# Kernel optimization log

Hardware: AMD Instinct MI355X
Metric: run time of the kernel (lower is better)

## Reference

```python
import jax, jax.numpy as jnp
import numpy as np

BS, T, N, M, P = 1024, 128, 128, 256, 256


def _lstm_cell(xin, h, c, Wih, Whh, bih, bhh):
    # PyTorch LSTMCell: gates ordered i, f, g, o
    z = xin @ Wih.T + bih + h @ Whh.T + bhh
    i, f, g, o = jnp.split(z, 4, axis=1)
    i = jax.nn.sigmoid(i); f = jax.nn.sigmoid(f)
    g = jnp.tanh(g); o = jax.nn.sigmoid(o)
    c2 = f * c + i * g
    return o * jnp.tanh(c2), c2


def setup_inputs() -> dict:
    key = jax.random.key(0)
    ks = jax.random.split(key, 24)
    s = 0.05
    return {
        "x": jax.random.normal(ks[0], (BS, T, N), jnp.float32),
        "y_known": jax.random.normal(ks[1], (BS, T, 1), jnp.float32),
        "We": jax.random.normal(ks[2], (T, 2 * M), jnp.float32) * s,
        "Ue": jax.random.normal(ks[3], (T, T), jnp.float32) * s,
        "Ve": jax.random.normal(ks[4], (1, T), jnp.float32) * s,
        "Wih_e": jax.random.normal(ks[5], (4 * M, N), jnp.float32) * s,
        "Whh_e": jax.random.normal(ks[6], (4 * M, M), jnp.float32) * s,
        "bih_e": jax.random.normal(ks[7], (4 * M,), jnp.float32) * s,
        "bhh_e": jax.random.normal(ks[8], (4 * M,), jnp.float32) * s,
        "Wd": jax.random.normal(ks[9], (M, 2 * P), jnp.float32) * s,
        "Ud": jax.random.normal(ks[10], (M, M), jnp.float32) * s,
        "Vd": jax.random.normal(ks[11], (1, M), jnp.float32) * s,
        "Wih_d": jax.random.normal(ks[12], (4 * P, 1), jnp.float32) * s,
        "Whh_d": jax.random.normal(ks[13], (4 * P, P), jnp.float32) * s,
        "bih_d": jax.random.normal(ks[14], (4 * P,), jnp.float32) * s,
        "bhh_d": jax.random.normal(ks[15], (4 * P,), jnp.float32) * s,
        "Wt": jax.random.normal(ks[16], (1, M + 1), jnp.float32) * s,
        "bt": jax.random.normal(ks[17], (1,), jnp.float32) * s,
        "W1": jax.random.normal(ks[18], (P, P + M), jnp.float32) * s,
        "b1": jax.random.normal(ks[19], (P,), jnp.float32) * s,
        "W2": jax.random.normal(ks[20], (1, P), jnp.float32) * s,
        "b2": jax.random.normal(ks[21], (1,), jnp.float32) * s,
    }


def reference(x, y_known, We, Ue, Ve, Wih_e, Whh_e, bih_e, bhh_e,
              Wd, Ud, Vd, Wih_d, Whh_d, bih_d, bhh_d,
              Wt, bt, W1, b1, W2, b2):
    bs, Tl, n = x.shape
    m = Whh_e.shape[1]
    p = Whh_d.shape[1]

    # ---- encoder (input attention) ----
    # U_e(x.permute(0,2,1)): loop-invariant, hoisted. (bs, n, T)
    Ux = jnp.einsum('btn,st->bns', x, Ue)

    def enc_step(carry, _):
        h, s = carry
        hs = jnp.concatenate([h, s], axis=1)            # (bs, 2m)
        ohs = hs @ We.T                                  # (bs, T)
        tanh_sum = jnp.tanh(ohs[:, None, :] + Ux)        # (bs, n, T)
        e = jnp.einsum('bnt,t->bn', tanh_sum, Ve[0])     # (bs, n)
        alpha = jax.nn.softmax(e, axis=1)
        xt = alpha * e                                   # faithful quirk: alpha * e_t
        h2, s2 = _lstm_cell(xt, h, s, Wih_e, Whh_e, bih_e, bhh_e)
        return (h2, s2), h2

    z = jnp.zeros((bs, m), x.dtype)
    _, h_all = jax.lax.scan(enc_step, (z, z), None, length=Tl)
    x1 = jnp.transpose(h_all, (1, 2, 0))                 # (bs, m, T)

    # ---- decoder (temporal attention) ----
    Udx = jnp.einsum('bmt,km->btk', x1, Ud)              # (bs, T, m)

    def dec_step(carry, yt):
        d, s, _ = carry
        ds = jnp.concatenate([d, s], axis=1)             # (bs, 2p)
        ods = ds @ Wd.T                                   # (bs, m)
        tanh_sum = jnp.tanh(ods[:, None, :] + Udx)        # (bs, T, m)
        l = jnp.einsum('btm,m->bt', tanh_sum, Vd[0])      # (bs, T)
        beta = jax.nn.softmax(l, axis=1)
        c = jnp.einsum('bt,bmt->bm', beta, x1)            # (bs, m)
        y_tilde = jnp.concatenate([yt, c], axis=1) @ Wt.T + bt  # (bs, 1)
        d2, s2 = _lstm_cell(y_tilde, d, s, Wih_d, Whh_d, bih_d, bhh_d)
        return (d2, s2, c), None

    zp = jnp.zeros((bs, p), x.dtype)
    zc = jnp.zeros((bs, m), x.dtype)
    (d, _, c), _ = jax.lax.scan(dec_step, (zp, zp, zc),
                                jnp.transpose(y_known, (1, 0, 2)))
    out1 = jnp.concatenate([d, c], axis=1) @ W1.T + b1
    return out1 @ W2.T + b2
```

## Files before the change

kernel.cpp:

```cpp
#include <hip/hip_runtime.h>


typedef unsigned int   uint;
typedef unsigned short ushort;
typedef _Float16 h2v __attribute__((ext_vector_type(2)));

#define O_WEH     0u
#define O_WENCH   32768u
#define O_WDH     229376u
#define O_WHHDH   294912u
#define O_UDT     425984u
#define O_UET     491520u
#define O_W1T     507904u
#define O_BENC    638976u
#define O_BDEC    640000u
#define W_FLOATS  641024u
#define O_X1H     641024u
#define O_BUF     17418240u
#define WS_FLOATS 34195456u

#define C2E 2.8853900817779268f
#define L2E 1.4426950408889634f

#define FMA4(acc, s, w) \
  acc.x = fmaf((s), (w).x, acc.x); \
  acc.y = fmaf((s), (w).y, acc.y); \
  acc.z = fmaf((s), (w).z, acc.z); \
  acc.w = fmaf((s), (w).w, acc.w);

union H2U { uint u; h2v h; _Float16 hs[2]; };

__device__ __forceinline__ float fdot2u(uint w, uint s, float acc) {
  H2U a; a.u = w; H2U b; b.u = s;
  return __builtin_amdgcn_fdot2(a.h, b.h, acc, false);
}
__device__ __forceinline__ uint pk2(float lo, float hi) {
  H2U v; v.hs[0] = (_Float16)lo; v.hs[1] = (_Float16)hi; return v.u;
}
__device__ __forceinline__ float h2lo(uint u) { H2U v; v.u = u; return (float)v.hs[0]; }
__device__ __forceinline__ float h2hi(uint u) { H2U v; v.u = u; return (float)v.hs[1]; }

__device__ __forceinline__ float fsig(float x) {
  return __builtin_amdgcn_rcpf(1.f + __builtin_amdgcn_exp2f(-L2E * x));
}
__device__ __forceinline__ float fth(float x) {
  float r = __builtin_amdgcn_rcpf(1.f + __builtin_amdgcn_exp2f(C2E * x));
  return fmaf(-2.f, r, 1.f);
}

__device__ __forceinline__ float grp4_sum(float v, float* red) {
  #pragma unroll
  for (int o = 32; o > 0; o >>= 1) v += __shfl_xor(v, o);
  __syncthreads();
  int w = threadIdx.x >> 6;
  if ((threadIdx.x & 63) == 0) red[w] = v;
  __syncthreads();
  int wb = w & 4;
  return (red[wb] + red[wb + 1]) + (red[wb + 2] + red[wb + 3]);
}
__device__ __forceinline__ float grp4_max(float v, float* red) {
  #pragma unroll
  for (int o = 32; o > 0; o >>= 1) v = fmaxf(v, __shfl_xor(v, o));
  __syncthreads();
  int w = threadIdx.x >> 6;
  if ((threadIdx.x & 63) == 0) red[w] = v;
  __syncthreads();
  int wb = w & 4;
  return fmaxf(fmaxf(red[wb], red[wb + 1]), fmaxf(red[wb + 2], red[wb + 3]));
}

__global__ __launch_bounds__(256) void prep_k(
    const float* __restrict__ We,    const float* __restrict__ Wih_e,
    const float* __restrict__ Whh_e, const float* __restrict__ Wd,
    const float* __restrict__ Whh_d, const float* __restrict__ W1,
    const float* __restrict__ Ud,    const float* __restrict__ Ue,
    const float* __restrict__ bih_e, const float* __restrict__ bhh_e,
    const float* __restrict__ bih_d, const float* __restrict__ bhh_d,
    float* __restrict__ ws)
{
  uint* wsu = (uint*)ws;
  unsigned idx = blockIdx.x * 256u + threadIdx.x;
  if (idx >= W_FLOATS) return;
  if (idx < 32768u) {
    unsigned kp = idx >> 7, j = idx & 127u;
    wsu[O_WEH + idx] = pk2(We[j * 512u + 2u*kp], We[j * 512u + 2u*kp + 1u]);
  } else if (idx < 229376u) {
    unsigned rel = idx - 32768u;
    unsigned kp = rel >> 10, j = rel & 1023u;
    float v0, v1;
    if (kp < 64u) { v0 = Wih_e[j * 128u + 2u*kp];          v1 = Wih_e[j * 128u + 2u*kp + 1u]; }
    else { unsigned k0 = 2u*(kp - 64u); v0 = Whh_e[j * 256u + k0]; v1 = Whh_e[j * 256u + k0 + 1u]; }
    wsu[O_WENCH + rel] = pk2(v0, v1);
  } else if (idx < 294912u) {
    unsigned rel = idx - 229376u;
    unsigned kp = rel >> 8, kk = rel & 255u;
    wsu[O_WDH + rel] = pk2(Wd[kk * 512u + 2u*kp], Wd[kk * 512u + 2u*kp + 1u]);
  } else if (idx < 425984u) {
    unsigned rel = idx - 294912u;
    unsigned kp = rel >> 10, j = rel & 1023u;
    wsu[O_WHHDH + rel] = pk2(Whh_d[j * 256u + 2u*kp], Whh_d[j * 256u + 2u*kp + 1u]);
  } else if (idx < 491520u) {
    unsigned rel = idx - 425984u;
    unsigned m = rel >> 8, k = rel & 255u;
    ws[O_UDT + rel] = Ud[k * 256u + m];
  } else if (idx < 507904u) {
    unsigned rel = idx - 491520u;
    unsigned t = rel >> 7, s = rel & 127u;
    ws[O_UET + rel] = Ue[s * 128u + t];
  } else if (idx < 638976u) {
    unsigned rel = idx - 507904u;
    unsigned k = rel >> 8, q = rel & 255u;
    ws[O_W1T + rel] = W1[q * 512u + k];
  } else if (idx < 640000u) {
    unsigned rel = idx - 638976u;
    ws[O_BENC + rel] = bih_e[rel] + bhh_e[rel];
  } else {
    unsigned rel = idx - 640000u;
    ws[O_BDEC + rel] = bih_d[rel] + bhh_d[rel];
  }
}

__global__ __launch_bounds__(256) void ux_k(
    const float* __restrict__ x, const float* __restrict__ UeT,
    uint* __restrict__ UxU)
{
  __shared__ float xs[128][32];
  const int b  = blockIdx.x >> 2;
  const int i0 = (blockIdx.x & 3) * 32;
  const int tid = threadIdx.x;
  for (int idx = tid; idx < 4096; idx += 256) {
    int t = idx >> 5, il = idx & 31;
    xs[t][il] = x[(size_t)b * 16384 + t * 128 + i0 + il];
  }
  __syncthreads();
  const int sl = tid & 31;
  const int ig = tid >> 5;
  const float4* UeT4 = (const float4*)UeT;
  float4 acc[4];
  #pragma unroll
  for (int ii = 0; ii < 4; ++ii) acc[ii] = make_float4(0.f, 0.f, 0.f, 0.f);
  for (int t = 0; t < 128; ++t) {
    float4 w = UeT4[t * 32 + sl];
    #pragma unroll
    for (int ii = 0; ii < 4; ++ii) {
      float a = xs[t][ig + 8 * ii];
      FMA4(acc[ii], a, w);
    }
  }
  uint2* U2 = (uint2*)UxU;
  #pragma unroll
  for (int ii = 0; ii < 4; ++ii) {
    int i_loc = i0 + ig + 8 * ii;
    uint2 pk;
    pk.x = pk2(acc[ii].x, acc[ii].y);
    pk.y = pk2(acc[ii].z, acc[ii].w);
    U2[((size_t)b * 128 + i_loc) * 32 + sl] = pk;
  }
}

__global__ __launch_bounds__(256) void udx_k(
    const uint* __restrict__ x1hU, const float* __restrict__ UdT,
    uint* __restrict__ UdxU)
{
  __shared__ float xs[32][256];
  const int b  = blockIdx.x >> 2;
  const int t0 = (blockIdx.x & 3) * 32;
  const int tid = threadIdx.x;
  const uint4* x14 = (const uint4*)x1hU + (size_t)b * 4096;
  for (int it = 0; it < 4; ++it) {
    int f = tid + it * 256;
    int tl = f >> 5, mq = f & 31;
    uint4 u = x14[(size_t)(t0 + tl) * 32 + mq];
    float* d = &xs[tl][mq * 8];
    d[0] = h2lo(u.x); d[1] = h2hi(u.x); d[2] = h2lo(u.y); d[3] = h2hi(u.y);
    d[4] = h2lo(u.z); d[5] = h2hi(u.z); d[6] = h2lo(u.w); d[7] = h2hi(u.w);
  }
  __syncthreads();
  const int kl = tid & 63;
  const int tg = tid >> 6;
  const float4* UdT4 = (const float4*)UdT;
  float4 acc[8];
  #pragma unroll
  for (int tt = 0; tt < 8; ++tt) acc[tt] = make_float4(0.f, 0.f, 0.f, 0.f);
  for (int m = 0; m < 256; ++m) {
    float4 w = UdT4[m * 64 + kl];
    #pragma unroll
    for (int tt = 0; tt < 8; ++tt) {
      float a = xs[tg + 4 * tt][m];
      FMA4(acc[tt], a, w);
    }
  }
  uint2* U2 = (uint2*)UdxU;
  #pragma unroll
  for (int tt = 0; tt < 8; ++tt) {
    uint2 pk;
    pk.x = pk2(acc[tt].x, acc[tt].y);
    pk.y = pk2(acc[tt].z, acc[tt].w);
    U2[((size_t)b * 128 + t0 + tg + 4 * tt) * 64 + kl] = pk;
  }
}

__global__ __launch_bounds__(512, 4) void encoder_k(
    const uint* __restrict__ WeH, const uint* __restrict__ WencH,
    const float* __restrict__ benc, const float* __restrict__ Ve,
    const uint* __restrict__ UxH, uint* __restrict__ x1hU)
{
  __shared__ uint stH[2][256];
  __shared__ uint xtH[2][64];
  __shared__ __align__(16) float part[4096];
  __shared__ float ohs2[2][128];
  __shared__ float xtT[128][2];
  __shared__ float bencS[1024];
  __shared__ float VeS[128];
  __shared__ float red[8];

  const int tid = threadIdx.x;
  const int b0 = blockIdx.x * 2;

  ((uint*)stH)[tid] = 0u;
  for (int i = tid; i < 1024; i += 512) bencS[i] = benc[i];
  if (tid < 128) VeS[tid] = Ve[tid];
  __syncthreads();

  float SVe = 0.f;
  #pragma unroll 8
  for (int s = 0; s < 128; ++s) SVe += VeS[s];

  const uint4* WeH4   = (const uint4*)WeH;
  const uint4* WencH4 = (const uint4*)WencH;
  float4* part4 = (float4*)part;

  const int rB = tid >> 8, iB = (tid >> 1) & 127, sh = tid & 1;
  const uint4* ux4 = (const uint4*)UxH + ((size_t)(b0 + rB) * 128 + iB) * 16 + sh * 8;

  float c_reg = 0.f;

  for (int step = 0; step < 128; ++step) {
    {
      const int j4 = tid & 31, ks = tid >> 5;
      float a0=0,a1=0,a2=0,a3=0,b0=0,b1=0,b2=0,b3=0;
      const int kb = ks * 16;
      #pragma unroll 4
      for (int kp = kb; kp < kb + 16; ++kp) {
        uint4 w = WeH4[kp * 32 + j4];
        uint s0 = stH[0][kp], s1 = stH[1][kp];
        a0 = fdot2u(w.x, s0, a0); a1 = fdot2u(w.y, s0, a1);
        a2 = fdot2u(w.z, s0, a2); a3 = fdot2u(w.w, s0, a3);
        b0 = fdot2u(w.x, s1, b0); b1 = fdot2u(w.y, s1, b1);
        b2 = fdot2u(w.z, s1, b2); b3 = fdot2u(w.w, s1, b3);
      }
      part4[(ks * 2 + 0) * 32 + j4] = make_float4(a0, a1, a2, a3);
      part4[(ks * 2 + 1) * 32 + j4] = make_float4(b0, b1, b2, b3);
    }
    __syncthreads();
    if (tid < 256) {
      const int r = tid >> 7, j = tid & 127;
      float acc = 0.f;
      #pragma unroll
      for (int ks = 0; ks < 16; ++ks) acc += part[(ks * 2 + r) * 128 + j];
      ohs2[r][j] = acc * C2E;
    }
    __syncthreads();
    float e_val;
    {
      float a0 = 0.f, a1 = 0.f, a2 = 0.f, a3 = 0.f;
      const float* oh = ohs2[rB];
      #pragma unroll 2
      for (int so = 0; so < 8; ++so) {
        uint4 u = ux4[so];
        const int s = sh * 64 + so * 8;
        a0 = fmaf(VeS[s+0], __builtin_amdgcn_rcpf(1.f + __builtin_amdgcn_exp2f(fmaf(C2E, h2lo(u.x), oh[s+0]))), a0);
        a1 = fmaf(VeS[s+1], __builtin_amdgcn_rcpf(1.f + __builtin_amdgcn_exp2f(fmaf(C2E, h2hi(u.x), oh[s+1]))), a1);
        a2 = fmaf(VeS[s+2], __builtin_amdgcn_rcpf(1.f + __builtin_amdgcn_exp2f(fmaf(C2E, h2lo(u.y), oh[s+2]))), a2);
        a3 = fmaf(VeS[s+3], __builtin_amdgcn_rcpf(1.f + __builtin_amdgcn_exp2f(fmaf(C2E, h2hi(u.y), oh[s+3]))), a3);
        a0 = fmaf(VeS[s+4], __builtin_amdgcn_rcpf(1.f + __builtin_amdgcn_exp2f(fmaf(C2E, h2lo(u.z), oh[s+4]))), a0);
        a1 = fmaf(VeS[s+5], __builtin_amdgcn_rcpf(1.f + __builtin_amdgcn_exp2f(fmaf(C2E, h2hi(u.z), oh[s+5]))), a1);
        a2 = fmaf(VeS[s+6], __builtin_amdgcn_rcpf(1.f + __builtin_amdgcn_exp2f(fmaf(C2E, h2lo(u.w), oh[s+6]))), a2);
        a3 = fmaf(VeS[s+7], __builtin_amdgcn_rcpf(1.f + __builtin_amdgcn_exp2f(fmaf(C2E, h2hi(u.w), oh[s+7]))), a3);
      }
      float r4 = (a0 + a1) + (a2 + a3);
      r4 += __shfl_xor(r4, 1);
      e_val = fmaf(-2.f, r4, SVe);
    }
    float mx = grp4_max(e_val, red);
    float p  = __builtin_amdgcn_exp2f(L2E * (e_val - mx));
    float sm = grp4_sum(sh == 0 ? p : 0.f, red);
    if (sh == 0) xtT[iB][rB] = p * __builtin_amdgcn_rcpf(sm) * e_val;
    __syncthreads();
    if (tid < 128) {
      const int r = tid >> 6, ii = tid & 63;
      xtH[r][ii] = pk2(xtT[2 * ii][r], xtT[2 * ii + 1][r]);
    }
    __syncthreads();
    {
      const int j4 = tid & 255, ks = tid >> 8;
      float a0=0,a1=0,a2=0,a3=0,b0=0,b1=0,b2=0,b3=0;
      if (ks == 0) {
        #pragma unroll 2
        for (int kp = 0; kp < 64; ++kp) {
          uint4 w = WencH4[kp * 256 + j4];
          uint s0 = xtH[0][kp], s1 = xtH[1][kp];
          a0 = fdot2u(w.x, s0, a0); a1 = fdot2u(w.y, s0, a1);
          a2 = fdot2u(w.z, s0, a2); a3 = fdot2u(w.w, s0, a3);
          b0 = fdot2u(w.x, s1, b0); b1 = fdot2u(w.y, s1, b1);
          b2 = fdot2u(w.z, s1, b2); b3 = fdot2u(w.w, s1, b3);
        }
        #pragma unroll 2
        for (int kp = 64; kp < 96; ++kp) {
          uint4 w = WencH4[kp * 256 + j4];
          uint s0 = stH[0][kp - 64], s1 = stH[1][kp - 64];
          a0 = fdot2u(w.x, s0, a0); a1 = fdot2u(w.y, s0, a1);
          a2 = fdot2u(w.z, s0, a2); a3 = fdot2u(w.w, s0, a3);
          b0 = fdot2u(w.x, s1, b0); b1 = fdot2u(w.y, s1, b1);
          b2 = fdot2u(w.z, s1, b2); b3 = fdot2u(w.w, s1, b3);
        }
      } else {
        #pragma unroll 2
        for (int kp = 96; kp < 192; ++kp) {
          uint4 w = WencH4[kp * 256 + j4];
          uint s0 = stH[0][kp - 64], s1 = stH[1][kp - 64];
          a0 = fdot2u(w.x, s0, a0); a1 = fdot2u(w.y, s0, a1);
          a2 = fdot2u(w.z, s0, a2); a3 = fdot2u(w.w, s0, a3);
          b0 = fdot2u(w.x, s1, b0); b1 = fdot2u(w.y, s1, b1);
          b2 = fdot2u(w.z, s1, b2); b3 = fdot2u(w.w, s1, b3);
        }
      }
      part4[(ks * 2 + 0) * 256 + j4] = make_float4(a0, a1, a2, a3);
      part4[(ks * 2 + 1) * 256 + j4] = make_float4(b0, b1, b2, b3);
    }
    __syncthreads();
    {
      const int r = tid >> 8, j = tid & 255;
      float z0 = bencS[j]       + part[r * 1024 + j]       + part[(2 + r) * 1024 + j];
      float z1 = bencS[256 + j] + part[r * 1024 + 256 + j] + part[(2 + r) * 1024 + 256 + j];
      float z2 = bencS[512 + j] + part[r * 1024 + 512 + j] + part[(2 + r) * 1024 + 512 + j];
      float z3 = bencS[768 + j] + part[r * 1024 + 768 + j] + part[(2 + r) * 1024 + 768 + j];
      float gi = fsig(z0), gf = fsig(z1), gg = fth(z2), go = fsig(z3);
      float c2 = fmaf(gf, c_reg, gi * gg);
      c_reg = c2;
      float h2 = go * fth(c2);
      float hn = __shfl_down(h2, 1);
      float cn = __shfl_down(c2, 1);
      if (!(j & 1)) {
        uint hp = pk2(h2, hn), cp = pk2(c2, cn);
        stH[r][j >> 1] = hp;
        stH[r][128 + (j >> 1)] = cp;
        x1hU[((size_t)(b0 + r) * 128 + step) * 128 + (j >> 1)] = hp;
      }
    }
    __syncthreads();
  }
}

__global__ __launch_bounds__(512, 4) void decoder_k(
    const uint* __restrict__ WdH, const uint* __restrict__ WhhdH,
    const float* __restrict__ W1T, const float* __restrict__ bdec,
    const float* __restrict__ Vd,  const float* __restrict__ WihD,
    const float* __restrict__ Wt,  const float* __restrict__ btp,
    const float* __restrict__ b1,  const float* __restrict__ W2,
    const float* __restrict__ b2p, const float* __restrict__ yk,
    const uint* __restrict__ UdxH, const uint* __restrict__ x1hU,
    float* __restrict__ out)
{
  __shared__ uint stH[2][256];
  __shared__ __align__(16) float part[4096];
  __shared__ float ods2[2][256];
  __shared__ float cT[256][2];
  __shared__ float betaT[128][2];
  __shared__ float wihdS[1024];
  __shared__ float bdecS[1024];
  __shared__ float VdS[256];
  __shared__ float yts[2];
  __shared__ float red[8];

  const int tid = threadIdx.x;
  const int b0 = blockIdx.x * 2;

  ((uint*)stH)[tid] = 0u;
  for (int i = tid; i < 1024; i += 512) { wihdS[i] = WihD[i]; bdecS[i] = bdec[i]; }
  if (tid < 256) VdS[tid] = Vd[tid];
  __syncthreads();

  float SVd = 0.f;
  #pragma unroll 8
  for (int k = 0; k < 256; ++k) SVd += VdS[k];

  const float bt0 = btp[0];
  const uint4*  WdH4   = (const uint4*)WdH;
  const uint4*  WhhdH4 = (const uint4*)WhhdH;
  const float4* W1T4   = (const float4*)W1T;
  float4* part4 = (float4*)part;

  const int rB = tid >> 8, tB = (tid >> 1) & 127, kh = tid & 1;
  const uint4* ud4 = (const uint4*)UdxH + ((size_t)(b0 + rB) * 128 + tB) * 32 + kh * 16;
  const int m8 = tid & 31, rb2 = (tid >> 5) & 1, ts = tid >> 6;
  const uint4* x14 = (const uint4*)x1hU + (size_t)(b0 + rb2) * 4096 + m8;

  float c_reg = 0.f;

  for (int step = 0; step < 128; ++step) {
    {
      const int j4 = tid & 63, ks = tid >> 6;
      float a0=0,a1=0,a2=0,a3=0,b0=0,b1=0,b2=0,b3=0;
      const int kb = ks * 32;
      #pragma unroll 4
      for (int kp = kb; kp < kb + 32; ++kp) {
        uint4 w = WdH4[kp * 64 + j4];
        uint s0 = stH[0][kp], s1 = stH[1][kp];
        a0 = fdot2u(w.x, s0, a0); a1 = fdot2u(w.y, s0, a1);
        a2 = fdot2u(w.z, s0, a2); a3 = fdot2u(w.w, s0, a3);
        b0 = fdot2u(w.x, s1, b0); b1 = fdot2u(w.y, s1, b1);
        b2 = fdot2u(w.z, s1, b2); b3 = fdot2u(w.w, s1, b3);
      }
      part4[(ks * 2 + 0) * 64 + j4] = make_float4(a0, a1, a2, a3);
      part4[(ks * 2 + 1) * 64 + j4] = make_float4(b0, b1, b2, b3);
    }
    __syncthreads();
    {
      const int r = tid >> 8, kk = tid & 255;
      float acc = 0.f;
      #pragma unroll
      for (int ks = 0; ks < 8; ++ks) acc += part[(ks * 2 + r) * 256 + kk];
      ods2[r][kk] = acc * C2E;
    }
    __syncthreads();
    float l_val;
    {
      float a0 = 0.f, a1 = 0.f, a2 = 0.f, a3 = 0.f;
      const float* od = ods2[rB];
      #pragma unroll 2
      for (int ko = 0; ko < 16; ++ko) {
        uint4 u = ud4[ko];
        const int k = kh * 128 + ko * 8;
        a0 = fmaf(VdS[k+0], __builtin_amdgcn_rcpf(1.f + __builtin_amdgcn_exp2f(fmaf(C2E, h2lo(u.x), od[k+0]))), a0);
        a1 = fmaf(VdS[k+1], __builtin_amdgcn_rcpf(1.f + __builtin_amdgcn_exp2f(fmaf(C2E, h2hi(u.x), od[k+1]))), a1);
        a2 = fmaf(VdS[k+2], __builtin_amdgcn_rcpf(1.f + __builtin_amdgcn_exp2f(fmaf(C2E, h2lo(u.y), od[k+2]))), a2);
        a3 = fmaf(VdS[k+3], __builtin_amdgcn_rcpf(1.f + __builtin_amdgcn_exp2f(fmaf(C2E, h2hi(u.y), od[k+3]))), a3);
        a0 = fmaf(VdS[k+4], __builtin_amdgcn_rcpf(1.f + __builtin_amdgcn_exp2f(fmaf(C2E, h2lo(u.z), od[k+4]))), a0);
        a1 = fmaf(VdS[k+5], __builtin_amdgcn_rcpf(1.f + __builtin_amdgcn_exp2f(fmaf(C2E, h2hi(u.z), od[k+5]))), a1);
        a2 = fmaf(VdS[k+6], __builtin_amdgcn_rcpf(1.f + __builtin_amdgcn_exp2f(fmaf(C2E, h2lo(u.w), od[k+6]))), a2);
        a3 = fmaf(VdS[k+7], __builtin_amdgcn_rcpf(1.f + __builtin_amdgcn_exp2f(fmaf(C2E, h2hi(u.w), od[k+7]))), a3);
      }
      float r4 = (a0 + a1) + (a2 + a3);
      r4 += __shfl_xor(r4, 1);
      l_val = fmaf(-2.f, r4, SVd);
    }
    float mx = grp4_max(l_val, red);
    float p  = __builtin_amdgcn_exp2f(L2E * (l_val - mx));
    float sm = grp4_sum(kh == 0 ? p : 0.f, red);
    if (kh == 0) betaT[tB][rB] = p * __builtin_amdgcn_rcpf(sm);
    __syncthreads();
    {
      float c[8];
      #pragma unroll
      for (int e = 0; e < 8; ++e) c[e] = 0.f;
      #pragma unroll 4
      for (int tt = 0; tt < 16; ++tt) {
        const int t = ts * 16 + tt;
        float bv = betaT[t][rb2];
        uint4 u = x14[(size_t)t * 32];
        c[0] = fmaf(bv, h2lo(u.x), c[0]); c[1] = fmaf(bv, h2hi(u.x), c[1]);
        c[2] = fmaf(bv, h2lo(u.y), c[2]); c[3] = fmaf(bv, h2hi(u.y), c[3]);
        c[4] = fmaf(bv, h2lo(u.z), c[4]); c[5] = fmaf(bv, h2hi(u.z), c[5]);
        c[6] = fmaf(bv, h2lo(u.w), c[6]); c[7] = fmaf(bv, h2hi(u.w), c[7]);
      }
      part4[(ts * 2 + rb2) * 64 + m8 * 2]     = make_float4(c[0], c[1], c[2], c[3]);
      part4[(ts * 2 + rb2) * 64 + m8 * 2 + 1] = make_float4(c[4], c[5], c[6], c[7]);
    }
    __syncthreads();
    {
      const int r = tid >> 8, m = tid & 255;
      float v = 0.f;
      #pragma unroll
      for (int t8 = 0; t8 < 8; ++t8) v += part[(t8 * 2 + r) * 256 + m];
      cT[m][r] = v;
    }
    __syncthreads();
    {
      const int r = tid >> 8, i = tid & 255;
      float pv = cT[i][r] * Wt[1 + i];
      float sum = grp4_sum(pv, red);
      if ((tid & 255) == 0) {
        yts[r] = sum + yk[(size_t)(b0 + r) * 128 + step] * Wt[0] + bt0;
      }
    }
    {
      const int j4 = tid & 255, ks = tid >> 8;
      float a0=0,a1=0,a2=0,a3=0,b0=0,b1=0,b2=0,b3=0;
      const int kb = ks * 64;
      #pragma unroll 2
      for (int kp = kb; kp < kb + 64; ++kp) {
        uint4 w = WhhdH4[kp * 256 + j4];
        uint s0 = stH[0][kp], s1 = stH[1][kp];
        a0 = fdot2u(w.x, s0, a0); a1 = fdot2u(w.y, s0, a1);
        a2 = fdot2u(w.z, s0, a2); a3 = fdot2u(w.w, s0, a3);
        b0 = fdot2u(w.x, s1, b0); b1 = fdot2u(w.y, s1, b1);
        b2 = fdot2u(w.z, s1, b2); b3 = fdot2u(w.w, s1, b3);
      }
      part4[(ks * 2 + 0) * 256 + j4] = make_float4(a0, a1, a2, a3);
      part4[(ks * 2 + 1) * 256 + j4] = make_float4(b0, b1, b2, b3);
    }
    __syncthreads();
    {
      const int r = tid >> 8, j = tid & 255;
      float yt = yts[r];
      float z0 = fmaf(yt, wihdS[j],       bdecS[j])       + part[r * 1024 + j]       + part[(2 + r) * 1024 + j];
      float z1 = fmaf(yt, wihdS[256 + j], bdecS[256 + j]) + part[r * 1024 + 256 + j] + part[(2 + r) * 1024 + 256 + j];
      float z2 = fmaf(yt, wihdS[512 + j], bdecS[512 + j]) + part[r * 1024 + 512 + j] + part[(2 + r) * 1024 + 512 + j];
      float z3 = fmaf(yt, wihdS[768 + j], bdecS[768 + j]) + part[r * 1024 + 768 + j] + part[(2 + r) * 1024 + 768 + j];
      float gi = fsig(z0), gf = fsig(z1), gg = fth(z2), go = fsig(z3);
      float c2 = fmaf(gf, c_reg, gi * gg);
      c_reg = c2;
      float d2 = go * fth(c2);
      float dn = __shfl_down(d2, 1);
      float cn = __shfl_down(c2, 1);
      if (!(j & 1)) {
        stH[r][j >> 1] = pk2(d2, dn);
        stH[r][128 + (j >> 1)] = pk2(c2, cn);
      }
    }
    __syncthreads();
  }
  {
    const int l = tid & 63, ks = tid >> 6;
    float a0=0,a1=0,a2=0,a3=0,b0=0,b1=0,b2=0,b3=0;
    const int kb = ks * 64;
    if (ks < 4) {
      for (int k = kb; k < kb + 64; ++k) {
        float4 w = W1T4[k * 64 + l];
        uint u0 = stH[0][k >> 1], u1 = stH[1][k >> 1];
        float d0 = (k & 1) ? h2hi(u0) : h2lo(u0);
        float d1 = (k & 1) ? h2hi(u1) : h2lo(u1);
        a0=fmaf(d0,w.x,a0); a1=fmaf(d0,w.y,a1); a2=fmaf(d0,w.z,a2); a3=fmaf(d0,w.w,a3);
        b0=fmaf(d1,w.x,b0); b1=fmaf(d1,w.y,b1); b2=fmaf(d1,w.z,b2); b3=fmaf(d1,w.w,b3);
      }
    } else {
      for (int k = kb; k < kb + 64; ++k) {
        float4 w = W1T4[k * 64 + l];
        float c0 = cT[k - 256][0], c1 = cT[k - 256][1];
        a0=fmaf(c0,w.x,a0); a1=fmaf(c0,w.y,a1); a2=fmaf(c0,w.z,a2); a3=fmaf(c0,w.w,a3);
        b0=fmaf(c1,w.x,b0); b1=fmaf(c1,w.y,b1); b2=fmaf(c1,w.z,b2); b3=fmaf(c1,w.w,b3);
      }
    }
    part4[(ks * 2 + 0) * 64 + l] = make_float4(a0, a1, a2, a3);
    part4[(ks * 2 + 1) * 64 + l] = make_float4(b0, b1, b2, b3);
  }
  __syncthreads();
  {
    const int r = tid >> 8, q = tid & 255;
    float o1 = b1[q];
    #pragma unroll
    for (int ks = 0; ks < 8; ++ks) o1 += part[(ks * 2 + r) * 256 + q];
    float pv = o1 * W2[q];
    float sum = grp4_sum(pv, red);
    if ((tid & 255) == 0) out[b0 + r] = sum + b2p[0];
  }
}

extern "C" void kernel_launch(void* const* d_in, const int* in_sizes, int n_in,
                              void* d_out, int out_size, void* d_ws, size_t ws_size,
                              hipStream_t stream)
{
  const float* x       = (const float*)d_in[0];
  const float* y_known = (const float*)d_in[1];
  const float* We      = (const float*)d_in[2];
  const float* Ue      = (const float*)d_in[3];
  const float* Ve      = (const float*)d_in[4];
  const float* Wih_e   = (const float*)d_in[5];
  const float* Whh_e   = (const float*)d_in[6];
  const float* bih_e   = (const float*)d_in[7];
  const float* bhh_e   = (const float*)d_in[8];
  const float* Wd      = (const float*)d_in[9];
  const float* Ud      = (const float*)d_in[10];
  const float* Vd      = (const float*)d_in[11];
  const float* Wih_d   = (const float*)d_in[12];
  const float* Whh_d   = (const float*)d_in[13];
  const float* bih_d   = (const float*)d_in[14];
  const float* bhh_d   = (const float*)d_in[15];
  const float* Wt      = (const float*)d_in[16];
  const float* bt      = (const float*)d_in[17];
  const float* W1      = (const float*)d_in[18];
  const float* b1      = (const float*)d_in[19];
  const float* W2      = (const float*)d_in[20];
  const float* b2      = (const float*)d_in[21];

  float* ws  = (float*)d_ws;
  float* out = (float*)d_out;
  if (ws_size < (size_t)WS_FLOATS * 4u) return;

  uint* wsu  = (uint*)ws;
  uint* x1hU = (uint*)(ws + O_X1H);
  uint* bufU = (uint*)(ws + O_BUF);

  prep_k<<<(W_FLOATS + 255) / 256, 256, 0, stream>>>(
      We, Wih_e, Whh_e, Wd, Whh_d, W1, Ud, Ue,
      bih_e, bhh_e, bih_d, bhh_d, ws);

  ux_k<<<4096, 256, 0, stream>>>(x, ws + O_UET, bufU);
  encoder_k<<<512, 512, 0, stream>>>(wsu + O_WEH, wsu + O_WENCH,
                                     ws + O_BENC, Ve, bufU, x1hU);
  udx_k<<<4096, 256, 0, stream>>>(x1hU, ws + O_UDT, bufU);
  decoder_k<<<512, 512, 0, stream>>>(wsu + O_WDH, wsu + O_WHHDH,
                                     ws + O_W1T, ws + O_BDEC, Vd, Wih_d,
                                     Wt, bt, b1, W2, b2, y_known,
                                     bufU, x1hU, out);
}
```

Before: 7.281 ms.

## Double encoder/decoder block threads and drop softmax max reduction

Encoder and decoder recurrent kernels now run with 1024 threads per block instead of 512. Every matvec and attention stage is re-split to give each thread half the work, with padded shared arrays to avoid bank conflicts. The softmax max-subtraction pass is removed, which saves one block-wide reduction per step but relies on the logits being small enough not to overflow exp. Several barrier pairs are merged, for example by fusing the context reduction with the y_tilde dot product. The cost is more partial-sum traffic through shared memory and more threads waiting at each barrier.

```diff
diff --git a/kernel.cpp b/kernel.cpp
--- a/kernel.cpp
+++ b/kernel.cpp
@@ -48,26 +48,11 @@
   return fmaf(-2.f, r, 1.f);
 }
 
-__device__ __forceinline__ float grp4_sum(float v, float* red) {
-  #pragma unroll
-  for (int o = 32; o > 0; o >>= 1) v += __shfl_xor(v, o);
-  __syncthreads();
-  int w = threadIdx.x >> 6;
-  if ((threadIdx.x & 63) == 0) red[w] = v;
-  __syncthreads();
-  int wb = w & 4;
-  return (red[wb] + red[wb + 1]) + (red[wb + 2] + red[wb + 3]);
-}
-__device__ __forceinline__ float grp4_max(float v, float* red) {
-  #pragma unroll
-  for (int o = 32; o > 0; o >>= 1) v = fmaxf(v, __shfl_xor(v, o));
-  __syncthreads();
-  int w = threadIdx.x >> 6;
-  if ((threadIdx.x & 63) == 0) red[w] = v;
-  __syncthreads();
-  int wb = w & 4;
-  return fmaxf(fmaxf(red[wb], red[wb + 1]), fmaxf(red[wb + 2], red[wb + 3]));
-}
+#define DOT8(w, s0, s1) { \
+  a0 = fdot2u(w.x, s0, a0); a1 = fdot2u(w.y, s0, a1); \
+  a2 = fdot2u(w.z, s0, a2); a3 = fdot2u(w.w, s0, a3); \
+  b0 = fdot2u(w.x, s1, b0); b1 = fdot2u(w.y, s1, b1); \
+  b2 = fdot2u(w.z, s1, b2); b3 = fdot2u(w.w, s1, b3); }
 
 __global__ __launch_bounds__(256) void prep_k(
     const float* __restrict__ We,    const float* __restrict__ Wih_e,
@@ -200,38 +185,36 @@
   }
 }
 
-__global__ __launch_bounds__(512, 4) void encoder_k(
+__global__ __launch_bounds__(1024, 8) void encoder_k(
     const uint* __restrict__ WeH, const uint* __restrict__ WencH,
     const float* __restrict__ benc, const float* __restrict__ Ve,
     const uint* __restrict__ UxH, uint* __restrict__ x1hU)
 {
   __shared__ uint stH[2][256];
   __shared__ uint xtH[2][64];
-  __shared__ __align__(16) float part[4096];
-  __shared__ float ohs2[2][128];
-  __shared__ float xtT[128][2];
+  __shared__ __align__(16) float part[8192];
+  __shared__ float ohs2[264];
   __shared__ float bencS[1024];
-  __shared__ float VeS[128];
-  __shared__ float red[8];
+  __shared__ float VeS[132];
+  __shared__ float red[16];
 
   const int tid = threadIdx.x;
   const int b0 = blockIdx.x * 2;
 
-  ((uint*)stH)[tid] = 0u;
-  for (int i = tid; i < 1024; i += 512) bencS[i] = benc[i];
-  if (tid < 128) VeS[tid] = Ve[tid];
+  if (tid < 512) ((uint*)stH)[tid] = 0u;
+  bencS[tid] = benc[tid];
+  if (tid < 128) VeS[tid + (tid >> 5)] = Ve[tid];
   __syncthreads();
 
   float SVe = 0.f;
-  #pragma unroll 8
-  for (int s = 0; s < 128; ++s) SVe += VeS[s];
+  for (int s = 0; s < 128; ++s) SVe += Ve[s];
 
   const uint4* WeH4   = (const uint4*)WeH;
   const uint4* WencH4 = (const uint4*)WencH;
   float4* part4 = (float4*)part;
 
-  const int rB = tid >> 8, iB = (tid >> 1) & 127, sh = tid & 1;
-  const uint4* ux4 = (const uint4*)UxH + ((size_t)(b0 + rB) * 128 + iB) * 16 + sh * 8;
+  const int sq = tid & 3, iB = (tid >> 2) & 127, rB = tid >> 9;
+  const uint4* ux4 = (const uint4*)UxH + ((size_t)(b0 + rB) * 128 + iB) * 16 + sq * 4;
 
   float c_reg = 0.f;
 
@@ -239,15 +222,12 @@
     {
       const int j4 = tid & 31, ks = tid >> 5;
       float a0=0,a1=0,a2=0,a3=0,b0=0,b1=0,b2=0,b3=0;
-      const int kb = ks * 16;
-      #pragma unroll 4
-      for (int kp = kb; kp < kb + 16; ++kp) {
+      const int kb = ks * 8;
+      #pragma unroll
+      for (int kp = kb; kp < kb + 8; ++kp) {
         uint4 w = WeH4[kp * 32 + j4];
         uint s0 = stH[0][kp], s1 = stH[1][kp];
-        a0 = fdot2u(w.x, s0, a0); a1 = fdot2u(w.y, s0, a1);
-        a2 = fdot2u(w.z, s0, a2); a3 = fdot2u(w.w, s0, a3);
-        b0 = fdot2u(w.x, s1, b0); b1 = fdot2u(w.y, s1, b1);
-        b2 = fdot2u(w.z, s1, b2); b3 = fdot2u(w.w, s1, b3);
+        DOT8(w, s0, s1);
       }
       part4[(ks * 2 + 0) * 32 + j4] = make_float4(a0, a1, a2, a3);
       part4[(ks * 2 + 1) * 32 + j4] = make_float4(b0, b1, b2, b3);
@@ -257,85 +237,81 @@
       const int r = tid >> 7, j = tid & 127;
       float acc = 0.f;
       #pragma unroll
-      for (int ks = 0; ks < 16; ++ks) acc += part[(ks * 2 + r) * 128 + j];
-      ohs2[r][j] = acc * C2E;
+      for (int ks = 0; ks < 32; ++ks) acc += part[(ks * 2 + r) * 128 + j];
+      ohs2[r * 132 + j + (j >> 5)] = acc * C2E;
     }
     __syncthreads();
     float e_val;
     {
       float a0 = 0.f, a1 = 0.f, a2 = 0.f, a3 = 0.f;
-      const float* oh = ohs2[rB];
+      const float* oh = ohs2 + rB * 132 + sq * 33;
+      const float* vp = VeS + sq * 33;
       #pragma unroll 2
-      for (int so = 0; so < 8; ++so) {
+      for (int so = 0; so < 4; ++so) {
         uint4 u = ux4[so];
-        const int s = sh * 64 + so * 8;
-        a0 = fmaf(VeS[s+0], __builtin_amdgcn_rcpf(1.f + __builtin_amdgcn_exp2f(fmaf(C2E, h2lo(u.x), oh[s+0]))), a0);
-        a1 = fmaf(VeS[s+1], __builtin_amdgcn_rcpf(1.f + __builtin_amdgcn_exp2f(fmaf(C2E, h2hi(u.x), oh[s+1]))), a1);
-        a2 = fmaf(VeS[s+2], __builtin_amdgcn_rcpf(1.f + __builtin_amdgcn_exp2f(fmaf(C2E, h2lo(u.y), oh[s+2]))), a2);
-        a3 = fmaf(VeS[s+3], __builtin_amdgcn_rcpf(1.f + __builtin_amdgcn_exp2f(fmaf(C2E, h2hi(u.y), oh[s+3]))), a3);
-        a0 = fmaf(VeS[s+4], __builtin_amdgcn_rcpf(1.f + __builtin_amdgcn_exp2f(fmaf(C2E, h2lo(u.z), oh[s+4]))), a0);
-        a1 = fmaf(VeS[s+5], __builtin_amdgcn_rcpf(1.f + __builtin_amdgcn_exp2f(fmaf(C2E, h2hi(u.z), oh[s+5]))), a1);
-        a2 = fmaf(VeS[s+6], __builtin_amdgcn_rcpf(1.f + __builtin_amdgcn_exp2f(fmaf(C2E, h2lo(u.w), oh[s+6]))), a2);
-        a3 = fmaf(VeS[s+7], __builtin_amdgcn_rcpf(1.f + __builtin_amdgcn_exp2f(fmaf(C2E, h2hi(u.w), oh[s+7]))), a3);
+        const int s = so * 8;
+        a0 = fmaf(vp[s+0], __builtin_amdgcn_rcpf(1.f + __builtin_amdgcn_exp2f(fmaf(C2E, h2lo(u.x), oh[s+0]))), a0);
+        a1 = fmaf(vp[s+1], __builtin_amdgcn_rcpf(1.f + __builtin_amdgcn_exp2f(fmaf(C2E, h2hi(u.x), oh[s+1]))), a1);
+        a2 = fmaf(vp[s+2], __builtin_amdgcn_rcpf(1.f + __builtin_amdgcn_exp2f(fmaf(C2E, h2lo(u.y), oh[s+2]))), a2);
+        a3 = fmaf(vp[s+3], __builtin_amdgcn_rcpf(1.f + __builtin_amdgcn_exp2f(fmaf(C2E, h2hi(u.y), oh[s+3]))), a3);
+        a0 = fmaf(vp[s+4], __builtin_amdgcn_rcpf(1.f + __builtin_amdgcn_exp2f(fmaf(C2E, h2lo(u.z), oh[s+4]))), a0);
+        a1 = fmaf(vp[s+5], __builtin_amdgcn_rcpf(1.f + __builtin_amdgcn_exp2f(fmaf(C2E, h2hi(u.z), oh[s+5]))), a1);
+        a2 = fmaf(vp[s+6], __builtin_amdgcn_rcpf(1.f + __builtin_amdgcn_exp2f(fmaf(C2E, h2lo(u.w), oh[s+6]))), a2);
+        a3 = fmaf(vp[s+7], __builtin_amdgcn_rcpf(1.f + __builtin_amdgcn_exp2f(fmaf(C2E, h2hi(u.w), oh[s+7]))), a3);
       }
       float r4 = (a0 + a1) + (a2 + a3);
       r4 += __shfl_xor(r4, 1);
+      r4 += __shfl_xor(r4, 2);
       e_val = fmaf(-2.f, r4, SVe);
     }
-    float mx = grp4_max(e_val, red);
-    float p  = __builtin_amdgcn_exp2f(L2E * (e_val - mx));
-    float sm = grp4_sum(sh == 0 ? p : 0.f, red);
-    if (sh == 0) xtT[iB][rB] = p * __builtin_amdgcn_rcpf(sm) * e_val;
-    __syncthreads();
-    if (tid < 128) {
-      const int r = tid >> 6, ii = tid & 63;
-      xtH[r][ii] = pk2(xtT[2 * ii][r], xtT[2 * ii + 1][r]);
+    {
+      float p  = __builtin_amdgcn_exp2f(L2E * e_val);
+      float ps = (sq == 0) ? p : 0.f;
+      #pragma unroll
+      for (int o = 1; o < 64; o <<= 1) ps += __shfl_xor(ps, o);
+      __syncthreads();
+      if ((tid & 63) == 0) red[tid >> 6] = ps;
+      __syncthreads();
+      const int base = (tid >> 6) & 8;
+      float sm = ((red[base+0]+red[base+1])+(red[base+2]+red[base+3]))
+               + ((red[base+4]+red[base+5])+(red[base+6]+red[base+7]));
+      float xt = p * __builtin_amdgcn_rcpf(sm) * e_val;
+      float xn = __shfl_down(xt, 4);
+      if ((tid & 7) == 0) xtH[rB][iB >> 1] = pk2(xt, xn);
     }
     __syncthreads();
     {
       const int j4 = tid & 255, ks = tid >> 8;
       float a0=0,a1=0,a2=0,a3=0,b0=0,b1=0,b2=0,b3=0;
-      if (ks == 0) {
-        #pragma unroll 2
-        for (int kp = 0; kp < 64; ++kp) {
-          uint4 w = WencH4[kp * 256 + j4];
-          uint s0 = xtH[0][kp], s1 = xtH[1][kp];
-          a0 = fdot2u(w.x, s0, a0); a1 = fdot2u(w.y, s0, a1);
-          a2 = fdot2u(w.z, s0, a2); a3 = fdot2u(w.w, s0, a3);
-          b0 = fdot2u(w.x, s1, b0); b1 = fdot2u(w.y, s1, b1);
-          b2 = fdot2u(w.z, s1, b2); b3 = fdot2u(w.w, s1, b3);
-        }
-        #pragma unroll 2
-        for (int kp = 64; kp < 96; ++kp) {
-          uint4 w = WencH4[kp * 256 + j4];
-          uint s0 = stH[0][kp - 64], s1 = stH[1][kp - 64];
-          a0 = fdot2u(w.x, s0, a0); a1 = fdot2u(w.y, s0, a1);
-          a2 = fdot2u(w.z, s0, a2); a3 = fdot2u(w.w, s0, a3);
-          b0 = fdot2u(w.x, s1, b0); b1 = fdot2u(w.y, s1, b1);
-          b2 = fdot2u(w.z, s1, b2); b3 = fdot2u(w.w, s1, b3);
-        }
-      } else {
-        #pragma unroll 2
-        for (int kp = 96; kp < 192; ++kp) {
-          uint4 w = WencH4[kp * 256 + j4];
-          uint s0 = stH[0][kp - 64], s1 = stH[1][kp - 64];
-          a0 = fdot2u(w.x, s0, a0); a1 = fdot2u(w.y, s0, a1);
-          a2 = fdot2u(w.z, s0, a2); a3 = fdot2u(w.w, s0, a3);
-          b0 = fdot2u(w.x, s1, b0); b1 = fdot2u(w.y, s1, b1);
-          b2 = fdot2u(w.z, s1, b2); b3 = fdot2u(w.w, s1, b3);
-        }
+      const int kb = ks * 48;
+      const int xe = (kb + 48 < 64) ? kb + 48 : 64;
+      for (int kp = kb; kp < xe; ++kp) {
+        uint4 w = WencH4[kp * 256 + j4];
+        uint s0 = xtH[0][kp], s1 = xtH[1][kp];
+        DOT8(w, s0, s1);
+      }
+      const int h0 = (kb > 64) ? kb : 64;
+      for (int kp = h0; kp < kb + 48; ++kp) {
+        uint4 w = WencH4[kp * 256 + j4];
+        uint s0 = stH[0][kp - 64], s1 = stH[1][kp - 64];
+        DOT8(w, s0, s1);
       }
       part4[(ks * 2 + 0) * 256 + j4] = make_float4(a0, a1, a2, a3);
       part4[(ks * 2 + 1) * 256 + j4] = make_float4(b0, b1, b2, b3);
     }
     __syncthreads();
-    {
+    if (tid < 512) {
       const int r = tid >> 8, j = tid & 255;
-      float z0 = bencS[j]       + part[r * 1024 + j]       + part[(2 + r) * 1024 + j];
-      float z1 = bencS[256 + j] + part[r * 1024 + 256 + j] + part[(2 + r) * 1024 + 256 + j];
-      float z2 = bencS[512 + j] + part[r * 1024 + 512 + j] + part[(2 + r) * 1024 + 512 + j];
-      float z3 = bencS[768 + j] + part[r * 1024 + 768 + j] + part[(2 + r) * 1024 + 768 + j];
-      float gi = fsig(z0), gf = fsig(z1), gg = fth(z2), go = fsig(z3);
+      float z[4];
+      #pragma unroll
+      for (int g = 0; g < 4; ++g) {
+        const int jg = g * 256 + j;
+        float z_ = bencS[jg];
+        #pragma unroll
+        for (int ks = 0; ks < 4; ++ks) z_ += part[(ks * 2 + r) * 1024 + jg];
+        z[g] = z_;
+      }
+      float gi = fsig(z[0]), gf = fsig(z[1]), gg = fth(z[2]), go = fsig(z[3]);
       float c2 = fmaf(gf, c_reg, gi * gg);
       c_reg = c2;
       float h2 = go * fth(c2);
@@ -352,7 +328,7 @@
   }
 }
 
-__global__ __launch_bounds__(512, 4) void decoder_k(
+__global__ __launch_bounds__(1024, 8) void decoder_k(
     const uint* __restrict__ WdH, const uint* __restrict__ WhhdH,
     const float* __restrict__ W1T, const float* __restrict__ bdec,
     const float* __restrict__ Vd,  const float* __restrict__ WihD,
@@ -363,152 +339,163 @@
     float* __restrict__ out)
 {
   __shared__ uint stH[2][256];
-  __shared__ __align__(16) float part[4096];
-  __shared__ float ods2[2][256];
-  __shared__ float cT[256][2];
-  __shared__ float betaT[128][2];
+  __shared__ __align__(16) float part[8192];
+  __shared__ float ods2[520];
+  __shared__ float cT[512];
+  __shared__ float betaS[256];
   __shared__ float wihdS[1024];
   __shared__ float bdecS[1024];
-  __shared__ float VdS[256];
+  __shared__ float VdS[260];
   __shared__ float yts[2];
-  __shared__ float red[8];
+  __shared__ float red[16];
 
   const int tid = threadIdx.x;
   const int b0 = blockIdx.x * 2;
 
-  ((uint*)stH)[tid] = 0u;
-  for (int i = tid; i < 1024; i += 512) { wihdS[i] = WihD[i]; bdecS[i] = bdec[i]; }
-  if (tid < 256) VdS[tid] = Vd[tid];
+  if (tid < 512) ((uint*)stH)[tid] = 0u;
+  wihdS[tid] = WihD[tid];
+  bdecS[tid] = bdec[tid];
+  if (tid < 256) VdS[tid + (tid >> 6)] = Vd[tid];
   __syncthreads();
 
   float SVd = 0.f;
-  #pragma unroll 8
-  for (int k = 0; k < 256; ++k) SVd += VdS[k];
-
-  const float bt0 = btp[0];
+  for (int k = 0; k < 256; ++k) SVd += Vd[k];
+
+  const float bt0 = btp[0], Wt0 = Wt[0];
   const uint4*  WdH4   = (const uint4*)WdH;
   const uint4*  WhhdH4 = (const uint4*)WhhdH;
   const float4* W1T4   = (const float4*)W1T;
   float4* part4 = (float4*)part;
 
-  const int rB = tid >> 8, tB = (tid >> 1) & 127, kh = tid & 1;
-  const uint4* ud4 = (const uint4*)UdxH + ((size_t)(b0 + rB) * 128 + tB) * 32 + kh * 16;
-  const int m8 = tid & 31, rb2 = (tid >> 5) & 1, ts = tid >> 6;
-  const uint4* x14 = (const uint4*)x1hU + (size_t)(b0 + rb2) * 4096 + m8;
+  const int kq = tid & 3, tB = (tid >> 2) & 127, rB = tid >> 9;
+  const uint4* ud4 = (const uint4*)UdxH + ((size_t)(b0 + rB) * 128 + tB) * 32 + kq * 8;
+  const int mc = tid & 63, rb2 = (tid >> 6) & 1, ts = tid >> 7;
+  const uint2* x12 = (const uint2*)x1hU + (size_t)(b0 + rb2) * 8192 + mc;
 
   float c_reg = 0.f;
 
   for (int step = 0; step < 128; ++step) {
     {
       const int j4 = tid & 63, ks = tid >> 6;
+      float a0=0,a1=0,a2=0,a3=0,b0=0,b1=0,b2=0,b3=0;
+      const int kb = ks * 16;
+      #pragma unroll 4
+      for (int kp = kb; kp < kb + 16; ++kp) {
+        uint4 w = WdH4[kp * 64 + j4];
+        uint s0 = stH[0][kp], s1 = stH[1][kp];
+        DOT8(w, s0, s1);
+      }
+      part4[(ks * 2 + 0) * 64 + j4] = make_float4(a0, a1, a2, a3);
+      part4[(ks * 2 + 1) * 64 + j4] = make_float4(b0, b1, b2, b3);
+    }
+    __syncthreads();
+    if (tid < 512) {
+      const int r = tid >> 8, kk = tid & 255;
+      float acc = 0.f;
+      #pragma unroll
+      for (int ks = 0; ks < 16; ++ks) acc += part[(ks * 2 + r) * 256 + kk];
+      ods2[r * 260 + kk + (kk >> 6)] = acc * C2E;
+    }
+    __syncthreads();
+    float l_val;
+    {
+      float a0 = 0.f, a1 = 0.f, a2 = 0.f, a3 = 0.f;
+      const float* od = ods2 + rB * 260 + kq * 65;
+      const float* vp = VdS + kq * 65;
+      #pragma unroll 2
+      for (int ko = 0; ko < 8; ++ko) {
+        uint4 u = ud4[ko];
+        const int k = ko * 8;
+        a0 = fmaf(vp[k+0], __builtin_amdgcn_rcpf(1.f + __builtin_amdgcn_exp2f(fmaf(C2E, h2lo(u.x), od[k+0]))), a0);
+        a1 = fmaf(vp[k+1], __builtin_amdgcn_rcpf(1.f + __builtin_amdgcn_exp2f(fmaf(C2E, h2hi(u.x), od[k+1]))), a1);
+        a2 = fmaf(vp[k+2], __builtin_amdgcn_rcpf(1.f + __builtin_amdgcn_exp2f(fmaf(C2E, h2lo(u.y), od[k+2]))), a2);
+        a3 = fmaf(vp[k+3], __builtin_amdgcn_rcpf(1.f + __builtin_amdgcn_exp2f(fmaf(C2E, h2hi(u.y), od[k+3]))), a3);
+        a0 = fmaf(vp[k+4], __builtin_amdgcn_rcpf(1.f + __builtin_amdgcn_exp2f(fmaf(C2E, h2lo(u.z), od[k+4]))), a0);
+        a1 = fmaf(vp[k+5], __builtin_amdgcn_rcpf(1.f + __builtin_amdgcn_exp2f(fmaf(C2E, h2hi(u.z), od[k+5]))), a1);
+        a2 = fmaf(vp[k+6], __builtin_amdgcn_rcpf(1.f + __builtin_amdgcn_exp2f(fmaf(C2E, h2lo(u.w), od[k+6]))), a2);
+        a3 = fmaf(vp[k+7], __builtin_amdgcn_rcpf(1.f + __builtin_amdgcn_exp2f(fmaf(C2E, h2hi(u.w), od[k+7]))), a3);
+      }
+      float r4 = (a0 + a1) + (a2 + a3);
+      r4 += __shfl_xor(r4, 1);
+      r4 += __shfl_xor(r4, 2);
+      l_val = fmaf(-2.f, r4, SVd);
+    }
+    {
+      float p  = __builtin_amdgcn_exp2f(L2E * l_val);
+      float ps = (kq == 0) ? p : 0.f;
+      #pragma unroll
+      for (int o = 1; o < 64; o <<= 1) ps += __shfl_xor(ps, o);
+      __syncthreads();
+      if ((tid & 63) == 0) red[tid >> 6] = ps;
+      __syncthreads();
+      const int base = (tid >> 6) & 8;
+      float sm = ((red[base+0]+red[base+1])+(red[base+2]+red[base+3]))
+               + ((red[base+4]+red[base+5])+(red[base+6]+red[base+7]));
+      if (kq == 0) betaS[rB * 128 + tB] = p * __builtin_amdgcn_rcpf(sm);
+    }
+    __syncthreads();
+    {
+      float c0 = 0.f, c1 = 0.f, c2 = 0.f, c3 = 0.f;
+      const float* bS = betaS + rb2 * 128;
+      #pragma unroll 4
+      for (int tt = 0; tt < 16; ++tt) {
+        const int t = ts * 16 + tt;
+        float bv = bS[t];
+        uint2 u = x12[(size_t)t * 64];
+        c0 = fmaf(bv, h2lo(u.x), c0); c1 = fmaf(bv, h2hi(u.x), c1);
+        c2 = fmaf(bv, h2lo(u.y), c2); c3 = fmaf(bv, h2hi(u.y), c3);
+      }
+      part4[(ts * 2 + rb2) * 64 + mc] = make_float4(c0, c1, c2, c3);
+    }
+    __syncthreads();
+    {
+      float pv = 0.f;
+      if (tid < 512) {
+        const int r = tid >> 8, m = tid & 255;
+        float v = 0.f;
+        #pragma unroll
+        for (int t8 = 0; t8 < 8; ++t8) v += part[(t8 * 2 + r) * 256 + m];
+        cT[m * 2 + r] = v;
+        pv = v * Wt[1 + m];
+      }
+      #pragma unroll
+      for (int o = 1; o < 64; o <<= 1) pv += __shfl_xor(pv, o);
+      __syncthreads();
+      if ((tid & 63) == 0) red[tid >> 6] = pv;
+      __syncthreads();
+      if ((tid & 255) == 0 && tid < 512) {
+        const int r = tid >> 8, base = r * 4;
+        float s = (red[base] + red[base+1]) + (red[base+2] + red[base+3]);
+        yts[r] = s + yk[(size_t)(b0 + r) * 128 + step] * Wt0 + bt0;
+      }
+    }
+    {
+      const int j4 = tid & 255, ks = tid >> 8;
       float a0=0,a1=0,a2=0,a3=0,b0=0,b1=0,b2=0,b3=0;
       const int kb = ks * 32;
       #pragma unroll 4
       for (int kp = kb; kp < kb + 32; ++kp) {
-        uint4 w = WdH4[kp * 64 + j4];
-        uint s0 = stH[0][kp], s1 = stH[1][kp];
-        a0 = fdot2u(w.x, s0, a0); a1 = fdot2u(w.y, s0, a1);
-        a2 = fdot2u(w.z, s0, a2); a3 = fdot2u(w.w, s0, a3);
-        b0 = fdot2u(w.x, s1, b0); b1 = fdot2u(w.y, s1, b1);
-        b2 = fdot2u(w.z, s1, b2); b3 = fdot2u(w.w, s1, b3);
-      }
-      part4[(ks * 2 + 0) * 64 + j4] = make_float4(a0, a1, a2, a3);
-      part4[(ks * 2 + 1) * 64 + j4] = make_float4(b0, b1, b2, b3);
-    }
-    __syncthreads();
-    {
-      const int r = tid >> 8, kk = tid & 255;
-      float acc = 0.f;
-      #pragma unroll
-      for (int ks = 0; ks < 8; ++ks) acc += part[(ks * 2 + r) * 256 + kk];
-      ods2[r][kk] = acc * C2E;
-    }
-    __syncthreads();
-    float l_val;
-    {
-      float a0 = 0.f, a1 = 0.f, a2 = 0.f, a3 = 0.f;
-      const float* od = ods2[rB];
-      #pragma unroll 2
-      for (int ko = 0; ko < 16; ++ko) {
-        uint4 u = ud4[ko];
-        const int k = kh * 128 + ko * 8;
-        a0 = fmaf(VdS[k+0], __builtin_amdgcn_rcpf(1.f + __builtin_amdgcn_exp2f(fmaf(C2E, h2lo(u.x), od[k+0]))), a0);
-        a1 = fmaf(VdS[k+1], __builtin_amdgcn_rcpf(1.f + __builtin_amdgcn_exp2f(fmaf(C2E, h2hi(u.x), od[k+1]))), a1);
-        a2 = fmaf(VdS[k+2], __builtin_amdgcn_rcpf(1.f + __builtin_amdgcn_exp2f(fmaf(C2E, h2lo(u.y), od[k+2]))), a2);
-        a3 = fmaf(VdS[k+3], __builtin_amdgcn_rcpf(1.f + __builtin_amdgcn_exp2f(fmaf(C2E, h2hi(u.y), od[k+3]))), a3);
-        a0 = fmaf(VdS[k+4], __builtin_amdgcn_rcpf(1.f + __builtin_amdgcn_exp2f(fmaf(C2E, h2lo(u.z), od[k+4]))), a0);
-        a1 = fmaf(VdS[k+5], __builtin_amdgcn_rcpf(1.f + __builtin_amdgcn_exp2f(fmaf(C2E, h2hi(u.z), od[k+5]))), a1);
-        a2 = fmaf(VdS[k+6], __builtin_amdgcn_rcpf(1.f + __builtin_amdgcn_exp2f(fmaf(C2E, h2lo(u.w), od[k+6]))), a2);
-        a3 = fmaf(VdS[k+7], __builtin_amdgcn_rcpf(1.f + __builtin_amdgcn_exp2f(fmaf(C2E, h2hi(u.w), od[k+7]))), a3);
-      }
-      float r4 = (a0 + a1) + (a2 + a3);
-      r4 += __shfl_xor(r4, 1);
-      l_val = fmaf(-2.f, r4, SVd);
-    }
-    float mx = grp4_max(l_val, red);
-    float p  = __builtin_amdgcn_exp2f(L2E * (l_val - mx));
-    float sm = grp4_sum(kh == 0 ? p : 0.f, red);
-    if (kh == 0) betaT[tB][rB] = p * __builtin_amdgcn_rcpf(sm);
-    __syncthreads();
-    {
-      float c[8];
-      #pragma unroll
-      for (int e = 0; e < 8; ++e) c[e] = 0.f;
-      #pragma unroll 4
-      for (int tt = 0; tt < 16; ++tt) {
-        const int t = ts * 16 + tt;
-        float bv = betaT[t][rb2];
-        uint4 u = x14[(size_t)t * 32];
-        c[0] = fmaf(bv, h2lo(u.x), c[0]); c[1] = fmaf(bv, h2hi(u.x), c[1]);
-        c[2] = fmaf(bv, h2lo(u.y), c[2]); c[3] = fmaf(bv, h2hi(u.y), c[3]);
-        c[4] = fmaf(bv, h2lo(u.z), c[4]); c[5] = fmaf(bv, h2hi(u.z), c[5]);
-        c[6] = fmaf(bv, h2lo(u.w), c[6]); c[7] = fmaf(bv, h2hi(u.w), c[7]);
-      }
-      part4[(ts * 2 + rb2) * 64 + m8 * 2]     = make_float4(c[0], c[1], c[2], c[3]);
-      part4[(ts * 2 + rb2) * 64 + m8 * 2 + 1] = make_float4(c[4], c[5], c[6], c[7]);
-    }
-    __syncthreads();
-    {
-      const int r = tid >> 8, m = tid & 255;
-      float v = 0.f;
-      #pragma unroll
-      for (int t8 = 0; t8 < 8; ++t8) v += part[(t8 * 2 + r) * 256 + m];
-      cT[m][r] = v;
-    }
-    __syncthreads();
-    {
-      const int r = tid >> 8, i = tid & 255;
-      float pv = cT[i][r] * Wt[1 + i];
-      float sum = grp4_sum(pv, red);
-      if ((tid & 255) == 0) {
-        yts[r] = sum + yk[(size_t)(b0 + r) * 128 + step] * Wt[0] + bt0;
-      }
-    }
-    {
-      const int j4 = tid & 255, ks = tid >> 8;
-      float a0=0,a1=0,a2=0,a3=0,b0=0,b1=0,b2=0,b3=0;
-      const int kb = ks * 64;
-      #pragma unroll 2
-      for (int kp = kb; kp < kb + 64; ++kp) {
         uint4 w = WhhdH4[kp * 256 + j4];
         uint s0 = stH[0][kp], s1 = stH[1][kp];
-        a0 = fdot2u(w.x, s0, a0); a1 = fdot2u(w.y, s0, a1);
-        a2 = fdot2u(w.z, s0, a2); a3 = fdot2u(w.w, s0, a3);
-        b0 = fdot2u(w.x, s1, b0); b1 = fdot2u(w.y, s1, b1);
-        b2 = fdot2u(w.z, s1, b2); b3 = fdot2u(w.w, s1, b3);
+        DOT8(w, s0, s1);
       }
       part4[(ks * 2 + 0) * 256 + j4] = make_float4(a0, a1, a2, a3);
       part4[(ks * 2 + 1) * 256 + j4] = make_float4(b0, b1, b2, b3);
     }
     __syncthreads();
-    {
+    if (tid < 512) {
       const int r = tid >> 8, j = tid & 255;
       float yt = yts[r];
-      float z0 = fmaf(yt, wihdS[j],       bdecS[j])       + part[r * 1024 + j]       + part[(2 + r) * 1024 + j];
-      float z1 = fmaf(yt, wihdS[256 + j], bdecS[256 + j]) + part[r * 1024 + 256 + j] + part[(2 + r) * 1024 + 256 + j];
-      float z2 = fmaf(yt, wihdS[512 + j], bdecS[512 + j]) + part[r * 1024 + 512 + j] + part[(2 + r) * 1024 + 512 + j];
-      float z3 = fmaf(yt, wihdS[768 + j], bdecS[768 + j]) + part[r * 1024 + 768 + j] + part[(2 + r) * 1024 + 768 + j];
-      float gi = fsig(z0), gf = fsig(z1), gg = fth(z2), go = fsig(z3);
+      float z[4];
+      #pragma unroll
+      for (int g = 0; g < 4; ++g) {
+        const int jg = g * 256 + j;
+        float z_ = fmaf(yt, wihdS[jg], bdecS[jg]);
+        #pragma unroll
+        for (int ks = 0; ks < 4; ++ks) z_ += part[(ks * 2 + r) * 1024 + jg];
+        z[g] = z_;
+      }
+      float gi = fsig(z[0]), gf = fsig(z[1]), gg = fth(z[2]), go = fsig(z[3]);
       float c2 = fmaf(gf, c_reg, gi * gg);
       c_reg = c2;
       float d2 = go * fth(c2);
@@ -524,9 +511,9 @@
   {
     const int l = tid & 63, ks = tid >> 6;
     float a0=0,a1=0,a2=0,a3=0,b0=0,b1=0,b2=0,b3=0;
-    const int kb = ks * 64;
-    if (ks < 4) {
-      for (int k = kb; k < kb + 64; ++k) {
+    const int kb = ks * 32;
+    if (ks < 8) {
+      for (int k = kb; k < kb + 32; ++k) {
         float4 w = W1T4[k * 64 + l];
         uint u0 = stH[0][k >> 1], u1 = stH[1][k >> 1];
         float d0 = (k & 1) ? h2hi(u0) : h2lo(u0);
@@ -535,9 +522,9 @@
         b0=fmaf(d1,w.x,b0); b1=fmaf(d1,w.y,b1); b2=fmaf(d1,w.z,b2); b3=fmaf(d1,w.w,b3);
       }
     } else {
-      for (int k = kb; k < kb + 64; ++k) {
+      for (int k = kb; k < kb + 32; ++k) {
         float4 w = W1T4[k * 64 + l];
-        float c0 = cT[k - 256][0], c1 = cT[k - 256][1];
+        float c0 = cT[(k - 256) * 2], c1 = cT[(k - 256) * 2 + 1];
         a0=fmaf(c0,w.x,a0); a1=fmaf(c0,w.y,a1); a2=fmaf(c0,w.z,a2); a3=fmaf(c0,w.w,a3);
         b0=fmaf(c1,w.x,b0); b1=fmaf(c1,w.y,b1); b2=fmaf(c1,w.z,b2); b3=fmaf(c1,w.w,b3);
       }
@@ -547,13 +534,22 @@
   }
   __syncthreads();
   {
-    const int r = tid >> 8, q = tid & 255;
+    const int q = tid & 255, r = tid >> 9;
     float o1 = b1[q];
     #pragma unroll
-    for (int ks = 0; ks < 8; ++ks) o1 += part[(ks * 2 + r) * 256 + q];
-    float pv = o1 * W2[q];
-    float sum = grp4_sum(pv, red);
-    if ((tid & 255) == 0) out[b0 + r] = sum + b2p[0];
+    for (int ks = 0; ks < 16; ++ks) o1 += part[(ks * 2 + r) * 256 + q];
+    float pv = ((tid >> 8) & 1) ? 0.f : o1 * W2[q];
+    #pragma unroll
+    for (int o = 1; o < 64; o <<= 1) pv += __shfl_xor(pv, o);
+    __syncthreads();
+    if ((tid & 63) == 0) red[tid >> 6] = pv;
+    __syncthreads();
+    if ((tid & 511) == 0) {
+      const int base = (tid >> 6) & 8;
+      float s = ((red[base+0]+red[base+1])+(red[base+2]+red[base+3]))
+              + ((red[base+4]+red[base+5])+(red[base+6]+red[base+7]));
+      out[b0 + r] = s + b2p[0];
+    }
   }
 }
 
@@ -597,11 +593,11 @@
       bih_e, bhh_e, bih_d, bhh_d, ws);
 
   ux_k<<<4096, 256, 0, stream>>>(x, ws + O_UET, bufU);
-  encoder_k<<<512, 512, 0, stream>>>(wsu + O_WEH, wsu + O_WENCH,
-                                     ws + O_BENC, Ve, bufU, x1hU);
+  encoder_k<<<512, 1024, 0, stream>>>(wsu + O_WEH, wsu + O_WENCH,
+                                      ws + O_BENC, Ve, bufU, x1hU);
   udx_k<<<4096, 256, 0, stream>>>(x1hU, ws + O_UDT, bufU);
-  decoder_k<<<512, 512, 0, stream>>>(wsu + O_WDH, wsu + O_WHHDH,
-                                     ws + O_W1T, ws + O_BDEC, Vd, Wih_d,
-                                     Wt, bt, b1, W2, b2, y_known,
-                                     bufU, x1hU, out);
-}
+  decoder_k<<<512, 1024, 0, stream>>>(wsu + O_WDH, wsu + O_WHHDH,
+                                      ws + O_W1T, ws + O_BDEC, Vd, Wih_d,
+                                      Wt, bt, b1, W2, b2, y_known,
+                                      bufU, x1hU, out);
+}
```

After: 9.228 ms. +26.8%, slower.
